# Kernel optimization log

Measured on AMD Instinct MI355X. Metric: run time of the kernel, lower is better.

The kernel has to match this reference:

```python
import jax, jax.numpy as jnp
import numpy as np
from jax import lax

EPS = 1e-5
PH = PW = 2  # patch size

def _bn(x, g, b, m, v):
    # eval-mode BatchNorm2d on NCHW
    scale = (g / jnp.sqrt(v + EPS))[None, :, None, None]
    return (x - m[None, :, None, None]) * scale + b[None, :, None, None]

def _gn1(x, g, b):
    # GroupNorm(num_groups=1): normalize over (C,P,N) per sample
    mu = x.mean(axis=(1, 2, 3), keepdims=True)
    var = x.var(axis=(1, 2, 3), keepdims=True)
    return (x - mu) / jnp.sqrt(var + EPS) * g[None, :, None, None] + b[None, :, None, None]

def _conv1x1(x, w, b=None):
    y = jnp.einsum('oc,bcpn->bopn', w, x)
    if b is not None:
        y = y + b[None, :, None, None]
    return y

def _silu(x):
    return x * jax.nn.sigmoid(x)

def _lin_attn(x, qkv_w, qkv_b, out_w, out_b, D):
    # x: [B, D, P, N]
    qkv = _conv1x1(x, qkv_w, qkv_b)            # [B, 2D+1, P, N]
    q = qkv[:, :1]                              # [B, 1, P, N]
    k = qkv[:, 1:1 + D]                         # [B, D, P, N]
    v = qkv[:, 1 + D:]                          # [B, D, P, N]
    scores = jax.nn.softmax(q, axis=-1)         # softmax over patches N
    ctx = jnp.sum(k * scores, axis=-1, keepdims=True)  # [B, D, P, 1]
    out = jax.nn.relu(v) * ctx
    return _conv1x1(out, out_w, out_b)

def reference(x, dw_w, dw_bn_g, dw_bn_b, dw_bn_m, dw_bn_v, pw_w,
              gn1_g, gn1_b, qkv_w, qkv_b, out_w, out_b,
              gn2_g, gn2_b, ffn1_w, ffn1_b, ffn2_w, ffn2_b,
              gnf_g, gnf_b, proj_w, proj_bn_g, proj_bn_b, proj_bn_m, proj_bn_v):
    B, C, H, W = x.shape
    D = pw_w.shape[0]
    L = gn1_g.shape[0]
    # local representation: depthwise 3x3 conv + BN + SiLU, then 1x1 to attn dim
    y = lax.conv_general_dilated(x, dw_w, (1, 1), 'SAME',
                                 feature_group_count=C,
                                 dimension_numbers=('NCHW', 'OIHW', 'NCHW'))
    y = _silu(_bn(y, dw_bn_g, dw_bn_b, dw_bn_m, dw_bn_v))
    y = _conv1x1(y, pw_w)                       # [B, D, H, W]
    # unfold to [B, D, P, N] (non-overlapping patches, torch F.unfold ordering)
    nH, nW = H // PH, W // PW
    p = y.reshape(B, D, nH, PH, nW, PW).transpose(0, 1, 3, 5, 2, 4).reshape(B, D, PH * PW, nH * nW)
    # global representation: L pre-norm linear-attention + FFN blocks
    for i in range(L):
        p = p + _lin_attn(_gn1(p, gn1_g[i], gn1_b[i]), qkv_w[i], qkv_b[i], out_w[i], out_b[i], D)
        h = _gn1(p, gn2_g[i], gn2_b[i])
        h = _silu(_conv1x1(h, ffn1_w[i], ffn1_b[i]))
        h = _conv1x1(h, ffn2_w[i], ffn2_b[i])
        p = p + h
    p = _gn1(p, gnf_g, gnf_b)
    # fold back to [B, D, H, W]
    y = p.reshape(B, D, PH, PW, nH, nW).transpose(0, 1, 4, 2, 5, 3).reshape(B, D, H, W)
    # projection back to in_channels: 1x1 conv + BN (no act)
    y = _conv1x1(y, proj_w)
    y = _bn(y, proj_bn_g, proj_bn_b, proj_bn_m, proj_bn_v)
    return y

def setup_inputs() -> dict:
    key = jax.random.key(0)
    ks = iter(jax.random.split(key, 40))
    def rn(shape, s=0.05):
        return jax.random.normal(next(ks), shape, jnp.float32) * s
    B, C, H, W, D, F, L = 16, 256, 64, 64, 256, 512, 2
    return dict(
        x=jax.random.normal(next(ks), (B, C, H, W), jnp.float32),
        dw_w=rn((C, 1, 3, 3), 0.2),
        dw_bn_g=jnp.ones((C,), jnp.float32), dw_bn_b=jnp.zeros((C,), jnp.float32),
        dw_bn_m=rn((C,), 0.01), dw_bn_v=jnp.ones((C,), jnp.float32),
        pw_w=rn((D, C)),
        gn1_g=jnp.ones((L, D), jnp.float32), gn1_b=jnp.zeros((L, D), jnp.float32),
        qkv_w=rn((L, 2 * D + 1, D)), qkv_b=jnp.zeros((L, 2 * D + 1), jnp.float32),
        out_w=rn((L, D, D)), out_b=jnp.zeros((L, D), jnp.float32),
        gn2_g=jnp.ones((L, D), jnp.float32), gn2_b=jnp.zeros((L, D), jnp.float32),
        ffn1_w=rn((L, F, D)), ffn1_b=jnp.zeros((L, F), jnp.float32),
        ffn2_w=rn((L, D, F)), ffn2_b=jnp.zeros((L, D), jnp.float32),
        gnf_g=jnp.ones((D,), jnp.float32), gnf_b=jnp.zeros((D,), jnp.float32),
        proj_w=rn((C, D)),
        proj_bn_g=jnp.ones((C,), jnp.float32), proj_bn_b=jnp.zeros((C,), jnp.float32),
        proj_bn_m=rn((C,), 0.01), proj_bn_v=jnp.ones((C,), jnp.float32),
    )
```

## Files before the change

### kernel.cpp

```cpp
#include <hip/hip_runtime.h>
#include <hip/hip_bf16.h>
#include <stdint.h>


#define B_    16
#define C_    256
#define D_    256
#define NPIX  4096
#define NE_PB 1048576

typedef __attribute__((ext_vector_type(8))) short  short8;
typedef __attribute__((ext_vector_type(4))) short  short4v;
typedef __attribute__((ext_vector_type(4))) float  f32x4;
typedef __attribute__((ext_vector_type(2))) float  f32x2;

__device__ __forceinline__ float b2f(short s){
  return __uint_as_float(((unsigned)(unsigned short)s) << 16);
}
__device__ __forceinline__ short f2b(float f){
  __bf16 h = (__bf16)f;
  return *(short*)&h;
}
__device__ __forceinline__ float silu_f(float x){
  float e = __builtin_amdgcn_exp2f(-1.44269504f * x);
  return x * __builtin_amdgcn_rcpf(1.f + e);
}

__device__ __forceinline__ void gld16(const short* g, short* l){
  __builtin_amdgcn_global_load_lds(
      (const __attribute__((address_space(1))) void*)g,
      (__attribute__((address_space(3))) void*)l, 16, 0, 0);
}

__device__ __forceinline__ int pi2pix(int n){
  int p = n >> 10, idx = n & 1023;
  int h = ((idx >> 5) << 1) | (p >> 1);
  int w = ((idx & 31) << 1) | (p & 1);
  return h*64 + w;
}
__device__ __forceinline__ int pix2pi(int pix){
  int h = pix >> 6, w = pix & 63;
  return ((h & 1)*2 + (w & 1))*1024 + (h >> 1)*32 + (w >> 1);
}

__global__ void cvt6_k(const float* __restrict__ s0, const float* __restrict__ s1,
                       const float* __restrict__ s2, const float* __restrict__ s3,
                       const float* __restrict__ s4, const float* __restrict__ s5,
                       const float* __restrict__ g1, const float* __restrict__ g2,
                       const float* __restrict__ gf,
                       short* __restrict__ dst, float* __restrict__ stats){
  const int i = blockIdx.x*256 + threadIdx.x;
  if (blockIdx.x == 0 && threadIdx.x < 160) stats[threadIdx.x] = 0.f;
  if (i >= 1049088) return;
  float v;
  if      (i <  65536){ v = s0[i]; }
  else if (i < 328192){ int j = i -  65536;
                        v = s1[j] * g1[(j/131328)*256 + (j & 255)]; }
  else if (i < 459264){ v = s2[i - 328192]; }
  else if (i < 721408){ int j = i - 459264;
                        v = s3[j] * g2[(j >> 17)*256 + (j & 255)]; }
  else if (i < 983552){ v = s4[i - 721408]; }
  else               { int j = i - 983552;
                        v = s5[j] * gf[j & 255]; }
  dst[i] = f2b(v);
}

__global__ void fold_k(const float* __restrict__ qkvw, const float* __restrict__ f1w,
                       const float* __restrict__ pjw,
                       const float* __restrict__ g1, const float* __restrict__ b1,
                       const float* __restrict__ g2, const float* __restrict__ b2,
                       const float* __restrict__ gf, const float* __restrict__ bf,
                       float* __restrict__ uv){
  const int row = blockIdx.x;
  const int l = threadIdx.x;
  const float* W; const float* g; const float* bb;
  if (row < 1026){ int layer = row/513, o = row - layer*513;
    W = qkvw + (size_t)(layer*513 + o)*256; g = g1 + layer*256; bb = b1 + layer*256; }
  else if (row < 2050){ int r2 = row - 1026; int layer = r2 >> 9, o = r2 & 511;
    W = f1w + (size_t)(layer*512 + o)*256; g = g2 + layer*256; bb = b2 + layer*256; }
  else { int o = row - 2050; W = pjw + (size_t)o*256; g = gf; bb = bf; }
  float u = 0.f, v = 0.f;
#pragma unroll
  for (int k = 0; k < 4; ++k){
    const int c = l + k*64;
    const float w = W[c];
    u += w * g[c]; v += w * bb[c];
  }
#pragma unroll
  for (int o = 32; o > 0; o >>= 1){ u += __shfl_down(u, o); v += __shfl_down(v, o); }
  if (l == 0){ uv[row*2] = u; uv[row*2+1] = v; }
}

__global__ __launch_bounds__(256)
void dwconv_k(const float* __restrict__ X, const float* __restrict__ W,
              const float* __restrict__ G, const float* __restrict__ Bb,
              const float* __restrict__ Mn, const float* __restrict__ Vr,
              short* __restrict__ O){
  const int c = blockIdx.x, b = blockIdx.y;
  const int t = threadIdx.x;
  __shared__ float xs[66][68];
  if (t < 132){ int r = (t >= 66) ? 65 : 0; int cc = (t >= 66) ? t-66 : t; xs[r][cc] = 0.f; }
  if (t < 128){ int r = 1 + (t & 63); int cc = (t >> 6) ? 65 : 0; xs[r][cc] = 0.f; }
  const float* xp = X + ((size_t)(b*C_ + c)) * NPIX;
#pragma unroll
  for (int it = 0; it < 4; ++it){
    const int idx = it*256 + t;
    const int row = idx >> 4, cq = idx & 15;
    f32x4 v = *(const f32x4*)&xp[row*64 + cq*4];
    xs[row+1][cq*4+1] = v.x; xs[row+1][cq*4+2] = v.y;
    xs[row+1][cq*4+3] = v.z; xs[row+1][cq*4+4] = v.w;
  }
  float wgt[9];
#pragma unroll
  for (int j = 0; j < 9; ++j) wgt[j] = W[c*9 + j];
  const float scale = G[c] * rsqrtf(Vr[c] + 1e-5f);
  const float mu = Mn[c], bb = Bb[c];
  __syncthreads();
  const int tr = t >> 4, tc = t & 15;
  float win[6][6];
#pragma unroll
  for (int dr = 0; dr < 6; ++dr){
    f32x4 a = *(const f32x4*)&xs[tr*4+dr][tc*4];
    f32x2 bq = *(const f32x2*)&xs[tr*4+dr][tc*4+4];
    win[dr][0] = a.x; win[dr][1] = a.y; win[dr][2] = a.z; win[dr][3] = a.w;
    win[dr][4] = bq.x; win[dr][5] = bq.y;
  }
  short* op = O + ((size_t)(b*C_ + c)) * NPIX;
#pragma unroll
  for (int jr = 0; jr < 4; ++jr){
    short4v o;
#pragma unroll
    for (int jc = 0; jc < 4; ++jc){
      float s = 0.f;
#pragma unroll
      for (int dh = 0; dh < 3; ++dh)
#pragma unroll
        for (int dw = 0; dw < 3; ++dw)
          s += win[jr+dh][jc+dw] * wgt[dh*3+dw];
      float y = (s - mu) * scale + bb;
      o[jc] = f2b(silu_f(y));
    }
    *(short4v*)&op[(tr*4+jr)*64 + tc*4] = o;
  }
}

__global__ void transpose_k(const short* __restrict__ I, short* __restrict__ O){
  const int s0 = blockIdx.x*64, c0 = blockIdx.y*64, b = blockIdx.z;
  const int t = threadIdx.x;
  __shared__ short tile[64][68];
  const int hi = t >> 4, lo = t & 15;
#pragma unroll
  for (int cy = 0; cy < 4; ++cy){
    const int cl = cy*16 + hi;
    short4v v = *(const short4v*)&I[((size_t)(b*C_ + c0 + cl))*NPIX + s0 + lo*4];
    tile[lo*4+0][cl] = v.x; tile[lo*4+1][cl] = v.y;
    tile[lo*4+2][cl] = v.z; tile[lo*4+3][cl] = v.w;
  }
  __syncthreads();
#pragma unroll
  for (int py = 0; py < 4; ++py){
    const int pl = py*16 + hi;
    short4v v = *(const short4v*)&tile[pl][lo*4];
    *(short4v*)&O[((size_t)(b*NPIX + s0 + pl))*C_ + c0 + lo*4] = v;
  }
}

template<int EPI, int K, int FOLD, int GATHER>
__global__ __launch_bounds__(256, 3)
void gemm_k(const short* __restrict__ Wt, const short* __restrict__ X,
            const int M,
            const float* __restrict__ bias,
            short* __restrict__ P,
            short* __restrict__ Obf,
            float* __restrict__ Of32,
            const float* __restrict__ bng, const float* __restrict__ bnb,
            const float* __restrict__ bnm, const float* __restrict__ bnv,
            float* __restrict__ st,
            const float* __restrict__ uv, const float* __restrict__ stIn)
{
  constexpr int S = K / 64;
  const int nt = blockIdx.x;
  const int ct = blockIdx.y;
  const int b  = blockIdx.z;
  const int tid = threadIdx.x;
  const int ln = tid & 63, wv = tid >> 6;
  const int wx = wv & 1;
  const int wy = wv >> 1;
  const int lr = ln & 15, lq = ln >> 4;
  const int rl = ln >> 3, sp = ln & 7;
  const int sw = sp ^ rl;
  const int ch8 = (tid & 15) * 8;

  __shared__ __align__(16) char smem[33824];
  short* As = (short*)smem;
  short* Xs = (short*)(smem + 16384);
  float* CT = (float*)smem;
  float* red = (float*)(smem + 33792);

  const short* Wp = Wt + (size_t)(ct*128)*K;
  const short* Xp = X + ((size_t)b*NPIX + (size_t)nt*128) * K;

  const short* gw[4]; const short* gx[4]; short* lw[4]; short* lx[4];
#pragma unroll
  for (int j = 0; j < 4; ++j){
    const int row = 32*wv + 8*j + rl;
    gw[j] = Wp + (size_t)row*K + sw*8;
    if constexpr (GATHER == 1)
      gx[j] = X + ((size_t)b*NPIX + pi2pix(nt*128 + row))*K + sw*8;
    else if constexpr (GATHER == 2)
      gx[j] = X + ((size_t)b*NPIX + pix2pi(nt*128 + row))*K + sw*8;
    else
      gx[j] = Xp + (size_t)row*K + sw*8;
    lw[j] = As + (4*wv + j)*512;
    lx[j] = Xs + (4*wv + j)*512;
  }

  short8 oldv[2][4];
  if constexpr (EPI == 2){
#pragma unroll
    for (int p = 0; p < 2; ++p)
#pragma unroll
      for (int it = 0; it < 4; ++it){
        const int pixL = it*16 + (tid >> 4);
        const size_t rowb = (size_t)b*NPIX + nt*128 + p*64 + pixL;
        oldv[p][it] = *(const short8*)&P[rowb*256 + ct*128 + ch8];
      }
  }

  f32x4 acc[4][4];
#pragma unroll
  for (int r = 0; r < 4; ++r)
#pragma unroll
    for (int c = 0; c < 4; ++c) acc[r][c] = (f32x4){0.f,0.f,0.f,0.f};

  for (int stp = 0; stp < S; ++stp){
    if (stp) __syncthreads();
#pragma unroll
    for (int j = 0; j < 4; ++j) gld16(gw[j] + stp*64, lw[j]);
#pragma unroll
    for (int j = 0; j < 4; ++j) gld16(gx[j] + stp*64, lx[j]);
    __syncthreads();
#pragma unroll
    for (int kk = 0; kk < 2; ++kk){
      const int seg = ((kk*4 + lq) ^ (lr & 7)) * 16;
      short8 aw[4], bx[4];
#pragma unroll
      for (int r = 0; r < 4; ++r)
        aw[r] = *(const short8*)((const char*)As + (wx*64 + r*16 + lr)*128 + seg);
#pragma unroll
      for (int c = 0; c < 4; ++c)
        bx[c] = *(const short8*)((const char*)Xs + (wy*64 + c*16 + lr)*128 + seg);
#pragma unroll
      for (int r = 0; r < 4; ++r)
#pragma unroll
        for (int c = 0; c < 4; ++c)
          acc[r][c] = __builtin_amdgcn_mfma_f32_16x16x32_bf16(aw[r], bx[c], acc[r][c], 0, 0, 0);
    }
  }

  float s_mul = 1.f;
  f32x4 be0 = (f32x4){0.f,0.f,0.f,0.f}, be1 = be0;
  if constexpr (EPI == 1 || EPI == 2 || EPI == 3){
    if constexpr (!FOLD){
      be0 = *(const f32x4*)&bias[ct*128 + ch8];
      be1 = *(const f32x4*)&bias[ct*128 + ch8 + 4];
    }
  }
  if constexpr (FOLD && EPI != 4){
    const float mean = stIn[b*2]   * (1.f/NE_PB);
    const float m2   = stIn[b*2+1] * (1.f/NE_PB);
    const float inv  = rsqrtf(m2 - mean*mean + 1e-5f);
    s_mul = inv;
    const float muinv = mean * inv;
    const float* up = &uv[(size_t)(ct*128 + ch8)*2];
#pragma unroll
    for (int k = 0; k < 4; ++k){
      f32x2 p0 = *(const f32x2*)&up[k*2];
      f32x2 p1 = *(const f32x2*)&up[8 + k*2];
      be0[k] += p0.y - muinv*p0.x;
      be1[k] += p1.y - muinv*p1.x;
    }
    if constexpr (EPI == 1 || EPI == 2 || EPI == 3){
      if (bias){
        f32x4 bb0 = *(const f32x4*)&bias[ct*128 + ch8];
        f32x4 bb1 = *(const f32x4*)&bias[ct*128 + ch8 + 4];
        be0.x += bb0.x; be0.y += bb0.y; be0.z += bb0.z; be0.w += bb0.w;
        be1.x += bb1.x; be1.y += bb1.y; be1.z += bb1.z; be1.w += bb1.w;
      }
    }
  }

  float sm = 0.f, ss = 0.f;

  if constexpr (EPI != 4){
#pragma unroll
    for (int p = 0; p < 2; ++p){
      __syncthreads();
      if (wy == p){
#pragma unroll
        for (int r = 0; r < 4; ++r)
#pragma unroll
          for (int c = 0; c < 4; ++c)
            *(f32x4*)&CT[(c*16 + lr)*132 + wx*64 + r*16 + lq*4] = acc[r][c];
      }
      __syncthreads();
#pragma unroll
      for (int it = 0; it < 4; ++it){
        const int pixL = it*16 + (tid >> 4);
        f32x4 v0 = *(const f32x4*)&CT[pixL*132 + ch8];
        f32x4 v1 = *(const f32x4*)&CT[pixL*132 + ch8 + 4];
        if constexpr (EPI != 0){
          v0.x = v0.x*s_mul + be0.x; v0.y = v0.y*s_mul + be0.y;
          v0.z = v0.z*s_mul + be0.z; v0.w = v0.w*s_mul + be0.w;
          v1.x = v1.x*s_mul + be1.x; v1.y = v1.y*s_mul + be1.y;
          v1.z = v1.z*s_mul + be1.z; v1.w = v1.w*s_mul + be1.w;
        }
        const int pixg = nt*128 + p*64 + pixL;
        const size_t rowb = (size_t)b*NPIX + pixg;
        if constexpr (EPI == 0){
          short8 o;
          o[0]=f2b(v0.x); o[1]=f2b(v0.y); o[2]=f2b(v0.z); o[3]=f2b(v0.w);
          o[4]=f2b(v1.x); o[5]=f2b(v1.y); o[6]=f2b(v1.z); o[7]=f2b(v1.w);
          *(short8*)&P[rowb*256 + ct*128 + ch8] = o;
          sm += v0.x+v0.y+v0.z+v0.w + v1.x+v1.y+v1.z+v1.w;
          ss += v0.x*v0.x+v0.y*v0.y+v0.z*v0.z+v0.w*v0.w
              + v1.x*v1.x+v1.y*v1.y+v1.z*v1.z+v1.w*v1.w;
        } else if constexpr (EPI == 2){
          short8 old = oldv[p][it];
          float n0 = b2f(old[0])+v0.x, n1 = b2f(old[1])+v0.y;
          float n2 = b2f(old[2])+v0.z, n3 = b2f(old[3])+v0.w;
          float n4 = b2f(old[4])+v1.x, n5 = b2f(old[5])+v1.y;
          float n6 = b2f(old[6])+v1.z, n7 = b2f(old[7])+v1.w;
          short8 o;
          o[0]=f2b(n0); o[1]=f2b(n1); o[2]=f2b(n2); o[3]=f2b(n3);
          o[4]=f2b(n4); o[5]=f2b(n5); o[6]=f2b(n6); o[7]=f2b(n7);
          *(short8*)&P[rowb*256 + ct*128 + ch8] = o;
          sm += n0+n1+n2+n3+n4+n5+n6+n7;
          ss += n0*n0+n1*n1+n2*n2+n3*n3+n4*n4+n5*n5+n6*n6+n7*n7;
        } else if constexpr (EPI == 1){
          short8 o;
          o[0]=f2b(v0.x); o[1]=f2b(v0.y); o[2]=f2b(v0.z); o[3]=f2b(v0.w);
          o[4]=f2b(v1.x); o[5]=f2b(v1.y); o[6]=f2b(v1.z); o[7]=f2b(v1.w);
          *(short8*)&Obf[rowb*(size_t)M + ct*128 + ch8] = o;
        } else {
          short8 o;
          o[0]=f2b(silu_f(v0.x)); o[1]=f2b(silu_f(v0.y));
          o[2]=f2b(silu_f(v0.z)); o[3]=f2b(silu_f(v0.w));
          o[4]=f2b(silu_f(v1.x)); o[5]=f2b(silu_f(v1.y));
          o[6]=f2b(silu_f(v1.z)); o[7]=f2b(silu_f(v1.w));
          *(short8*)&Obf[rowb*(size_t)M + ct*128 + ch8] = o;
        }
      }
    }
    if constexpr (EPI == 0 || EPI == 2){
#pragma unroll
      for (int o = 32; o > 0; o >>= 1){ sm += __shfl_down(sm, o); ss += __shfl_down(ss, o); }
      if (ln == 0){ red[wv*2] = sm; red[wv*2+1] = ss; }
      __syncthreads();
      if (tid == 0){
        atomicAdd(&st[b*2+0], red[0]+red[2]+red[4]+red[6]);
        atomicAdd(&st[b*2+1], red[1]+red[3]+red[5]+red[7]);
      }
    }
  } else {
    float muinv4 = 0.f;
    if constexpr (FOLD){
      const float mean = stIn[b*2]   * (1.f/NE_PB);
      const float m2   = stIn[b*2+1] * (1.f/NE_PB);
      const float inv  = rsqrtf(m2 - mean*mean + 1e-5f);
      s_mul = inv;
      muinv4 = mean * inv;
    }
#pragma unroll
    for (int p = 0; p < 2; ++p){
      __syncthreads();
      if (wx == p){
#pragma unroll
        for (int r = 0; r < 4; ++r)
#pragma unroll
          for (int c = 0; c < 4; ++c){
            const int pixL = wy*64 + c*16 + lr;
#pragma unroll
            for (int j = 0; j < 4; ++j)
              CT[(r*16 + lq*4 + j)*132 + pixL] = acc[r][c][j];
          }
      }
      __syncthreads();
#pragma unroll
      for (int it = 0; it < 8; ++it){
        const int idx = it*256 + tid;
        const int chL = idx >> 5, pq = (idx & 31)*4;
        const int chan = ct*128 + p*64 + chL;
        f32x4 v = *(const f32x4*)&CT[chL*132 + pq];
        const float sc = bng[chan] * rsqrtf(bnv[chan] + 1e-5f);
        const float mu = bnm[chan], bb = bnb[chan];
        float A = sc, Bc = -mu*sc + bb;
        if constexpr (FOLD){
          f32x2 uvp = *(const f32x2*)&uv[(size_t)chan*2];
          A = s_mul * sc;
          Bc = ((uvp.y - muinv4*uvp.x) - mu)*sc + bb;
        }
        f32x4 o;
        o.x = v.x*A + Bc; o.y = v.y*A + Bc;
        o.z = v.z*A + Bc; o.w = v.w*A + Bc;
        *(f32x4*)&Of32[((size_t)(b*C_ + chan))*NPIX + (size_t)nt*128 + pq] = o;
      }
    }
  }
}

__global__ void q_k(const short* __restrict__ P, const float* __restrict__ Wq,
                    const float* __restrict__ Gg, const float* __restrict__ Qb,
                    const float* __restrict__ uv, const float* __restrict__ stIn,
                    float* __restrict__ Q){
  const int lane = threadIdx.x & 63;
  const int pix = (blockIdx.x*256 + threadIdx.x) >> 6;
  const int b = pix >> 12;
  short4v u4 = *(const short4v*)&P[(size_t)pix*256 + lane*4];
  f32x4  w4 = *(const f32x4*)&Wq[lane*4];
  f32x4  g4 = *(const f32x4*)&Gg[lane*4];
  float s = b2f(u4.x)*w4.x*g4.x + b2f(u4.y)*w4.y*g4.y
          + b2f(u4.z)*w4.z*g4.z + b2f(u4.w)*w4.w*g4.w;
#pragma unroll
  for (int o = 32; o > 0; o >>= 1) s += __shfl_down(s, o);
  if (lane == 0){
    const float mean = stIn[b*2]   * (1.f/NE_PB);
    const float m2   = stIn[b*2+1] * (1.f/NE_PB);
    const float inv  = rsqrtf(m2 - mean*mean + 1e-5f);
    Q[pix] = inv*s + Qb[0] + uv[1] - inv*mean*uv[0];
  }
}

__global__ void softmax_k(const float* __restrict__ Q, float* __restrict__ S,
                          float* __restrict__ CT){
  const int bp = blockIdx.x;
  const int t = threadIdx.x;
  CT[bp*256 + t] = 0.f;
  float vals[4];
  float mx = -1e30f;
#pragma unroll
  for (int j = 0; j < 4; ++j){
    vals[j] = Q[bp*1024 + t + j*256];
    mx = fmaxf(mx, vals[j]);
  }
  __shared__ float red[4];
  const int lane = t & 63, wv = t >> 6;
#pragma unroll
  for (int o = 32; o > 0; o >>= 1) mx = fmaxf(mx, __shfl_down(mx, o));
  if (lane == 0) red[wv] = mx;
  __syncthreads();
  mx = fmaxf(fmaxf(red[0], red[1]), fmaxf(red[2], red[3]));
  __syncthreads();
  float sum = 0.f;
#pragma unroll
  for (int j = 0; j < 4; ++j){ vals[j] = expf(vals[j] - mx); sum += vals[j]; }
#pragma unroll
  for (int o = 32; o > 0; o >>= 1) sum += __shfl_down(sum, o);
  if (lane == 0) red[wv] = sum;
  __syncthreads();
  sum = red[0] + red[1] + red[2] + red[3];
  const float r = 1.f / sum;
#pragma unroll
  for (int j = 0; j < 4; ++j) S[bp*1024 + t + j*256] = vals[j]*r;
}

__global__ void ctx_k(const short* __restrict__ KV, const float* __restrict__ S,
                      float* __restrict__ CT){
  const int bp = blockIdx.x, ch = blockIdx.y;
  const int ln = threadIdx.x & 63, wv = threadIdx.x >> 6;
  const int j0 = ch*256 + wv*64;
  f32x4 acc = (f32x4){0.f,0.f,0.f,0.f};
  for (int jj = 0; jj < 64; jj += 4){
    f32x4 s4 = *(const f32x4*)&S[bp*1024 + j0 + jj];
#pragma unroll
    for (int u = 0; u < 4; ++u){
      short4v kv = *(const short4v*)&KV[((size_t)bp*1024 + j0 + jj + u)*512 + ln*4];
      const float s = s4[u];
      acc.x += b2f(kv.x)*s; acc.y += b2f(kv.y)*s;
      acc.z += b2f(kv.z)*s; acc.w += b2f(kv.w)*s;
    }
  }
  atomicAdd(&CT[bp*256 + ln*4 + 0], acc.x);
  atomicAdd(&CT[bp*256 + ln*4 + 1], acc.y);
  atomicAdd(&CT[bp*256 + ln*4 + 2], acc.z);
  atomicAdd(&CT[bp*256 + ln*4 + 3], acc.w);
}

__global__ void attn_in_k(const short* __restrict__ KV, const float* __restrict__ CT,
                          short* __restrict__ O){
  const size_t vid = (size_t)blockIdx.x*256 + threadIdx.x;
  const int c4 = (int)(vid & 63);
  const size_t r = vid >> 6;
  const int bp = (int)(r >> 10);
  short4v v4 = *(const short4v*)&KV[r*512 + 256 + c4*4];
  f32x4  cx = *(const f32x4*)&CT[bp*256 + c4*4];
  short4v o;
  o.x = f2b(fmaxf(b2f(v4.x), 0.f)*cx.x);
  o.y = f2b(fmaxf(b2f(v4.y), 0.f)*cx.y);
  o.z = f2b(fmaxf(b2f(v4.z), 0.f)*cx.z);
  o.w = f2b(fmaxf(b2f(v4.w), 0.f)*cx.w);
  *(short4v*)&O[r*256 + c4*4] = o;
}

extern "C" void kernel_launch(void* const* d_in, const int* in_sizes, int n_in,
                              void* d_out, int out_size, void* d_ws, size_t ws_size,
                              hipStream_t stream){
  const float* x      = (const float*)d_in[0];
  const float* dw_w   = (const float*)d_in[1];
  const float* dw_g   = (const float*)d_in[2];
  const float* dw_b   = (const float*)d_in[3];
  const float* dw_m   = (const float*)d_in[4];
  const float* dw_v   = (const float*)d_in[5];
  const float* pw_w   = (const float*)d_in[6];
  const float* gn1_g  = (const float*)d_in[7];
  const float* gn1_b  = (const float*)d_in[8];
  const float* qkv_w  = (const float*)d_in[9];
  const float* qkv_b  = (const float*)d_in[10];
  const float* out_w  = (const float*)d_in[11];
  const float* out_b  = (const float*)d_in[12];
  const float* gn2_g  = (const float*)d_in[13];
  const float* gn2_b  = (const float*)d_in[14];
  const float* ffn1_w = (const float*)d_in[15];
  const float* ffn1_b = (const float*)d_in[16];
  const float* ffn2_w = (const float*)d_in[17];
  const float* ffn2_b = (const float*)d_in[18];
  const float* gnf_g  = (const float*)d_in[19];
  const float* gnf_b  = (const float*)d_in[20];
  const float* proj_w = (const float*)d_in[21];
  const float* pbn_g  = (const float*)d_in[22];
  const float* pbn_b  = (const float*)d_in[23];
  const float* pbn_m  = (const float*)d_in[24];
  const float* pbn_v  = (const float*)d_in[25];
  float* out = (float*)d_out;

  uint8_t* w8 = (uint8_t*)d_ws;
  short* P     = (short*)(w8);
  short* bufA  = (short*)(w8 + 33554432);
  short* bufB  = (short*)(w8 + 67108864);
  short* wbase = (short*)(w8 + 134217728);
  short* w_pw  = wbase;
  short* w_qkv = wbase + 65536;
  short* w_out = wbase + 328192;
  short* w_f1  = wbase + 459264;
  short* w_f2  = wbase + 721408;
  short* w_pj  = wbase + 983552;
  float* qbuf  = (float*)(w8 + 136315904);
  float* scor  = (float*)(w8 + 136578048);
  float* ctxs  = (float*)(w8 + 136840192);
  float* stats = (float*)(w8 + 136905728);
  float* uvb   = (float*)(w8 + 136906368);

  cvt6_k<<<4098, 256, 0, stream>>>(pw_w, qkv_w, out_w, ffn1_w, ffn2_w, proj_w,
                                   gn1_g, gn2_g, gnf_g, wbase, stats);
  fold_k<<<2306, 64, 0, stream>>>(qkv_w, ffn1_w, proj_w,
                                  gn1_g, gn1_b, gn2_g, gn2_b, gnf_g, gnf_b, uvb);

  dwconv_k<<<dim3(256,16), 256, 0, stream>>>(x, dw_w, dw_g, dw_b, dw_m, dw_v, bufB);
  transpose_k<<<dim3(64,4,16), 256, 0, stream>>>(bufB, bufA);

  gemm_k<0,256,0,1><<<dim3(32,2,16), 256, 0, stream>>>(w_pw, bufA, 256, nullptr, P,
      nullptr, nullptr, nullptr, nullptr, nullptr, nullptr, stats + 0,
      nullptr, nullptr);

  for (int i = 0; i < 2; ++i){
    float* st1 = stats + (i == 0 ? 0 : 2)*32;
    q_k<<<16384, 256, 0, stream>>>(P, qkv_w + (size_t)i*513*256, gn1_g + i*256,
        qkv_b + i*513, uvb + (size_t)(i*513)*2, st1, qbuf);
    gemm_k<1,256,1,0><<<dim3(32,4,16), 256, 0, stream>>>(w_qkv + (i*513+1)*256, P, 512,
        qkv_b + i*513 + 1, nullptr, bufB, nullptr, nullptr, nullptr, nullptr, nullptr,
        nullptr, uvb + (size_t)(i*513+1)*2, st1);
    softmax_k<<<64, 256, 0, stream>>>(qbuf, scor, ctxs);
    ctx_k<<<dim3(64,4), 256, 0, stream>>>(bufB, scor, ctxs);
    attn_in_k<<<16384, 256, 0, stream>>>(bufB, ctxs, bufA);
    gemm_k<2,256,0,0><<<dim3(32,2,16), 256, 0, stream>>>(w_out + i*65536, bufA, 256,
        out_b + i*256, P, nullptr, nullptr, nullptr, nullptr, nullptr, nullptr,
        stats + (i == 0 ? 1 : 3)*32, nullptr, nullptr);
    float* st2 = stats + (i == 0 ? 1 : 3)*32;
    gemm_k<3,256,1,0><<<dim3(32,4,16), 256, 0, stream>>>(w_f1 + i*131072, P, 512,
        ffn1_b + i*512, nullptr, bufB, nullptr, nullptr, nullptr, nullptr, nullptr,
        nullptr, uvb + (size_t)(1026 + i*512)*2, st2);
    gemm_k<2,512,0,0><<<dim3(32,2,16), 256, 0, stream>>>(w_f2 + i*131072, bufB, 256,
        ffn2_b + i*256, P, nullptr, nullptr, nullptr, nullptr, nullptr, nullptr,
        stats + (i == 0 ? 2 : 4)*32, nullptr, nullptr);
  }

  gemm_k<4,256,1,2><<<dim3(32,2,16), 256, 0, stream>>>(w_pj, P, 256, nullptr,
      nullptr, nullptr, out, pbn_g, pbn_b, pbn_m, pbn_v, nullptr,
      uvb + (size_t)2050*2, stats + 4*32);

  (void)in_sizes; (void)n_in; (void)out_size; (void)ws_size;
}
```

Before: 580.0 us.

## Double-buffer GEMM LDS tiles with async global-to-LDS prefetch two stages ahead

Converts the GEMM main loop from a single LDS buffer, which loads and then syncs every K step, into a two-stage ping-pong buffer. The next tiles' global-to-LDS loads are issued while MFMAs run on the current buffer, coordinated with explicit vmcnt/lgkmcnt waits and s_barrier. The epilogue bias and GroupNorm fold computations are hoisted above the loop so their loads overlap too. LDS use doubles to 64KB and launch bounds drop to 2 blocks per CU, so occupancy falls in exchange for latency hiding.

After: 607.4 us. +4.7%, slower.

```diff
diff --git a/kernel.cpp b/kernel.cpp
--- a/kernel.cpp
+++ b/kernel.cpp
@@ -166,7 +166,7 @@
 }
 
 template<int EPI, int K, int FOLD, int GATHER>
-__global__ __launch_bounds__(256, 3)
+__global__ __launch_bounds__(256, 2)
 void gemm_k(const short* __restrict__ Wt, const short* __restrict__ X,
             const int M,
             const float* __restrict__ bias,
@@ -191,16 +191,14 @@
   const int sw = sp ^ rl;
   const int ch8 = (tid & 15) * 8;
 
-  __shared__ __align__(16) char smem[33824];
-  short* As = (short*)smem;
-  short* Xs = (short*)(smem + 16384);
+  __shared__ __align__(16) char smem[65568];
   float* CT = (float*)smem;
-  float* red = (float*)(smem + 33792);
+  float* red = (float*)(smem + 65536);
 
   const short* Wp = Wt + (size_t)(ct*128)*K;
   const short* Xp = X + ((size_t)b*NPIX + (size_t)nt*128) * K;
 
-  const short* gw[4]; const short* gx[4]; short* lw[4]; short* lx[4];
+  const short* gw[4]; const short* gx[4]; int lo4[4];
 #pragma unroll
   for (int j = 0; j < 4; ++j){
     const int row = 32*wv + 8*j + rl;
@@ -211,9 +209,17 @@
       gx[j] = X + ((size_t)b*NPIX + pix2pi(nt*128 + row))*K + sw*8;
     else
       gx[j] = Xp + (size_t)row*K + sw*8;
-    lw[j] = As + (4*wv + j)*512;
-    lx[j] = Xs + (4*wv + j)*512;
-  }
+    lo4[j] = (4*wv + j)*512;
+  }
+
+  auto stage = [&](int stp){
+    short* as = (short*)(smem + ((stp & 1) << 15));
+    short* xs = as + 8192;
+#pragma unroll
+    for (int j = 0; j < 4; ++j) gld16(gw[j] + stp*64, as + lo4[j]);
+#pragma unroll
+    for (int j = 0; j < 4; ++j) gld16(gx[j] + stp*64, xs + lo4[j]);
+  };
 
   short8 oldv[2][4];
   if constexpr (EPI == 2){
@@ -226,67 +232,77 @@
         oldv[p][it] = *(const short8*)&P[rowb*256 + ct*128 + ch8];
       }
   }
-
-  f32x4 acc[4][4];
-#pragma unroll
-  for (int r = 0; r < 4; ++r)
-#pragma unroll
-    for (int c = 0; c < 4; ++c) acc[r][c] = (f32x4){0.f,0.f,0.f,0.f};
-
-  for (int stp = 0; stp < S; ++stp){
-    if (stp) __syncthreads();
-#pragma unroll
-    for (int j = 0; j < 4; ++j) gld16(gw[j] + stp*64, lw[j]);
-#pragma unroll
-    for (int j = 0; j < 4; ++j) gld16(gx[j] + stp*64, lx[j]);
-    __syncthreads();
-#pragma unroll
-    for (int kk = 0; kk < 2; ++kk){
-      const int seg = ((kk*4 + lq) ^ (lr & 7)) * 16;
-      short8 aw[4], bx[4];
-#pragma unroll
-      for (int r = 0; r < 4; ++r)
-        aw[r] = *(const short8*)((const char*)As + (wx*64 + r*16 + lr)*128 + seg);
-#pragma unroll
-      for (int c = 0; c < 4; ++c)
-        bx[c] = *(const short8*)((const char*)Xs + (wy*64 + c*16 + lr)*128 + seg);
-#pragma unroll
-      for (int r = 0; r < 4; ++r)
-#pragma unroll
-        for (int c = 0; c < 4; ++c)
-          acc[r][c] = __builtin_amdgcn_mfma_f32_16x16x32_bf16(aw[r], bx[c], acc[r][c], 0, 0, 0);
-    }
-  }
-
   float s_mul = 1.f;
+  float muinv4 = 0.f;
   f32x4 be0 = (f32x4){0.f,0.f,0.f,0.f}, be1 = be0;
-  if constexpr (EPI == 1 || EPI == 2 || EPI == 3){
-    if constexpr (!FOLD){
-      be0 = *(const f32x4*)&bias[ct*128 + ch8];
-      be1 = *(const f32x4*)&bias[ct*128 + ch8 + 4];
-    }
-  }
-  if constexpr (FOLD && EPI != 4){
+  if constexpr ((EPI == 1 || EPI == 2 || EPI == 3) && !FOLD){
+    be0 = *(const f32x4*)&bias[ct*128 + ch8];
+    be1 = *(const f32x4*)&bias[ct*128 + ch8 + 4];
+  }
+  if constexpr (FOLD){
     const float mean = stIn[b*2]   * (1.f/NE_PB);
     const float m2   = stIn[b*2+1] * (1.f/NE_PB);
     const float inv  = rsqrtf(m2 - mean*mean + 1e-5f);
     s_mul = inv;
     const float muinv = mean * inv;
-    const float* up = &uv[(size_t)(ct*128 + ch8)*2];
-#pragma unroll
-    for (int k = 0; k < 4; ++k){
-      f32x2 p0 = *(const f32x2*)&up[k*2];
-      f32x2 p1 = *(const f32x2*)&up[8 + k*2];
-      be0[k] += p0.y - muinv*p0.x;
-      be1[k] += p1.y - muinv*p1.x;
-    }
-    if constexpr (EPI == 1 || EPI == 2 || EPI == 3){
-      if (bias){
-        f32x4 bb0 = *(const f32x4*)&bias[ct*128 + ch8];
-        f32x4 bb1 = *(const f32x4*)&bias[ct*128 + ch8 + 4];
-        be0.x += bb0.x; be0.y += bb0.y; be0.z += bb0.z; be0.w += bb0.w;
-        be1.x += bb1.x; be1.y += bb1.y; be1.z += bb1.z; be1.w += bb1.w;
-      }
+    muinv4 = muinv;
+    if constexpr (EPI != 4){
+      const float* up = &uv[(size_t)(ct*128 + ch8)*2];
+#pragma unroll
+      for (int k = 0; k < 4; ++k){
+        f32x2 p0 = *(const f32x2*)&up[k*2];
+        f32x2 p1 = *(const f32x2*)&up[8 + k*2];
+        be0[k] += p0.y - muinv*p0.x;
+        be1[k] += p1.y - muinv*p1.x;
+      }
+      if constexpr (EPI == 1 || EPI == 2 || EPI == 3){
+        if (bias){
+          f32x4 bb0 = *(const f32x4*)&bias[ct*128 + ch8];
+          f32x4 bb1 = *(const f32x4*)&bias[ct*128 + ch8 + 4];
+          be0.x += bb0.x; be0.y += bb0.y; be0.z += bb0.z; be0.w += bb0.w;
+          be1.x += bb1.x; be1.y += bb1.y; be1.z += bb1.z; be1.w += bb1.w;
+        }
+      }
+    }
+  }
+
+  f32x4 acc[4][4];
+#pragma unroll
+  for (int r = 0; r < 4; ++r)
+#pragma unroll
+    for (int c = 0; c < 4; ++c) acc[r][c] = (f32x4){0.f,0.f,0.f,0.f};
+
+  stage(0);
+  stage(1);
+  asm volatile("s_waitcnt vmcnt(8)" ::: "memory");
+  __builtin_amdgcn_s_barrier();
+
+  for (int stp = 0; stp < S; ++stp){
+    const char* asb = (const char*)smem + ((stp & 1) << 15);
+    const char* xsb = asb + 16384;
+#pragma unroll
+    for (int kk = 0; kk < 2; ++kk){
+      const int seg = ((kk*4 + lq) ^ (lr & 7)) * 16;
+      short8 aw[4], bx[4];
+#pragma unroll
+      for (int r = 0; r < 4; ++r)
+        aw[r] = *(const short8*)(asb + (wx*64 + r*16 + lr)*128 + seg);
+#pragma unroll
+      for (int c = 0; c < 4; ++c)
+        bx[c] = *(const short8*)(xsb + (wy*64 + c*16 + lr)*128 + seg);
+#pragma unroll
+      for (int r = 0; r < 4; ++r)
+#pragma unroll
+        for (int c = 0; c < 4; ++c)
+          acc[r][c] = __builtin_amdgcn_mfma_f32_16x16x32_bf16(aw[r], bx[c], acc[r][c], 0, 0, 0);
+    }
+    asm volatile("s_waitcnt lgkmcnt(0)" ::: "memory");
+    __builtin_amdgcn_s_barrier();
+    if (stp + 2 < S) stage(stp + 2);
+    if (stp + 1 < S){
+      if (stp + 2 < S) asm volatile("s_waitcnt vmcnt(8)" ::: "memory");
+      else             asm volatile("s_waitcnt vmcnt(0)" ::: "memory");
+      __builtin_amdgcn_s_barrier();
     }
   }
 
@@ -363,14 +379,6 @@
       }
     }
   } else {
-    float muinv4 = 0.f;
-    if constexpr (FOLD){
-      const float mean = stIn[b*2]   * (1.f/NE_PB);
-      const float m2   = stIn[b*2+1] * (1.f/NE_PB);
-      const float inv  = rsqrtf(m2 - mean*mean + 1e-5f);
-      s_mul = inv;
-      muinv4 = mean * inv;
-    }
 #pragma unroll
     for (int p = 0; p < 2; ++p){
       __syncthreads();
```

## Fuse FFN up and down projections into one kernel keeping hidden in LDS

Applied to the files above, without the earlier changes.

Replaces the two FFN GEMM launches with a single ffn_k kernel. Each block computes a 128-channel chunk of the hidden activation with GroupNorm folding and SiLU, stores it in shared memory, and immediately accumulates it into the down-projection, followed by the residual add and GroupNorm statistics. This removes the global-memory round trip of the 512-channel hidden tensor and one launch. The cost is fewer blocks (512 instead of 1024/2048), heavy register use from two accumulator sets, and a grid that may leave the GPU underfilled.

Result: slower. 603.4 us (+4.0%).

```diff
diff --git a/kernel.cpp b/kernel.cpp
--- a/kernel.cpp
+++ b/kernel.cpp
@@ -409,6 +409,195 @@
   }
 }
 
+__global__ __launch_bounds__(256, 2)
+void ffn_k(const short* __restrict__ Wf1, const short* __restrict__ Wf2,
+           const float* __restrict__ b1,  const float* __restrict__ b2,
+           short* __restrict__ P,
+           const float* __restrict__ uv, const float* __restrict__ stIn,
+           float* __restrict__ st)
+{
+  const int nt = blockIdx.x;
+  const int b  = blockIdx.y;
+  const int tid = threadIdx.x;
+  const int ln = tid & 63, wv = tid >> 6;
+  const int wx = wv & 1;
+  const int wy = wv >> 1;
+  const int lr = ln & 15, lq = ln >> 4;
+  const int rl = ln >> 3, sp = ln & 7;
+  const int sw = sp ^ rl;
+  const int ch8 = (tid & 15) * 8;
+
+  __shared__ __align__(16) char smem[65536];
+  short* As = (short*)smem;
+  short* Xs = (short*)(smem + 16384);
+  float* CT = (float*)smem;
+  float* red = (float*)(smem + 33792);
+
+  const short* Pt = P + ((size_t)b*NPIX + (size_t)nt*128) * 256;
+
+  int grow[4]; int lo4[4];
+#pragma unroll
+  for (int j = 0; j < 4; ++j){
+    grow[j] = 32*wv + 8*j + rl;
+    lo4[j] = (4*wv + j)*512;
+  }
+
+  const float mean = stIn[b*2]   * (1.f/NE_PB);
+  const float m2   = stIn[b*2+1] * (1.f/NE_PB);
+  const float inv  = rsqrtf(m2 - mean*mean + 1e-5f);
+  const float muinv = mean * inv;
+
+  f32x4 acc2[2][4][4];
+#pragma unroll
+  for (int d = 0; d < 2; ++d)
+#pragma unroll
+    for (int r = 0; r < 4; ++r)
+#pragma unroll
+      for (int c = 0; c < 4; ++c) acc2[d][r][c] = (f32x4){0.f,0.f,0.f,0.f};
+
+  for (int fc = 0; fc < 4; ++fc){
+    f32x4 acc1[4][4];
+#pragma unroll
+    for (int r = 0; r < 4; ++r)
+#pragma unroll
+      for (int c = 0; c < 4; ++c) acc1[r][c] = (f32x4){0.f,0.f,0.f,0.f};
+    const short* W1 = Wf1 + (size_t)(fc*128)*256;
+    for (int s = 0; s < 4; ++s){
+      __syncthreads();
+#pragma unroll
+      for (int j = 0; j < 4; ++j)
+        gld16(W1 + (size_t)grow[j]*256 + s*64 + sw*8, As + lo4[j]);
+#pragma unroll
+      for (int j = 0; j < 4; ++j)
+        gld16(Pt + (size_t)grow[j]*256 + s*64 + sw*8, Xs + lo4[j]);
+      __syncthreads();
+#pragma unroll
+      for (int kk = 0; kk < 2; ++kk){
+        const int seg = ((kk*4 + lq) ^ (lr & 7)) * 16;
+        short8 aw[4], bx[4];
+#pragma unroll
+        for (int r = 0; r < 4; ++r)
+          aw[r] = *(const short8*)((const char*)As + (wx*64 + r*16 + lr)*128 + seg);
+#pragma unroll
+        for (int c = 0; c < 4; ++c)
+          bx[c] = *(const short8*)((const char*)Xs + (wy*64 + c*16 + lr)*128 + seg);
+#pragma unroll
+        for (int r = 0; r < 4; ++r)
+#pragma unroll
+          for (int c = 0; c < 4; ++c)
+            acc1[r][c] = __builtin_amdgcn_mfma_f32_16x16x32_bf16(aw[r], bx[c], acc1[r][c], 0, 0, 0);
+      }
+    }
+    {
+      char* hkt = (char*)smem + 32768 + (wx << 14);
+      const int c16 = 2*0 + 0;  (void)c16;
+#pragma unroll
+      for (int r = 0; r < 4; ++r){
+        const int chanF = fc*128 + wx*64 + r*16 + lq*4;
+        f32x4 bb = *(const f32x4*)&b1[chanF];
+        f32x2 q0 = *(const f32x2*)&uv[(size_t)(chanF+0)*2];
+        f32x2 q1 = *(const f32x2*)&uv[(size_t)(chanF+1)*2];
+        f32x2 q2 = *(const f32x2*)&uv[(size_t)(chanF+2)*2];
+        f32x2 q3 = *(const f32x2*)&uv[(size_t)(chanF+3)*2];
+        f32x4 be;
+        be.x = bb.x + q0.y - muinv*q0.x;
+        be.y = bb.y + q1.y - muinv*q1.x;
+        be.z = bb.z + q2.y - muinv*q2.x;
+        be.w = bb.w + q3.y - muinv*q3.x;
+        const int ch16 = r*2 + (lq >> 1);
+        const int inner = (lq & 1)*8;
+#pragma unroll
+        for (int c = 0; c < 4; ++c){
+          const int pix = wy*64 + c*16 + lr;
+          f32x4 v = acc1[r][c];
+          short4v o;
+          o.x = f2b(silu_f(v.x*inv + be.x));
+          o.y = f2b(silu_f(v.y*inv + be.y));
+          o.z = f2b(silu_f(v.z*inv + be.z));
+          o.w = f2b(silu_f(v.w*inv + be.w));
+          *(short4v*)(hkt + pix*128 + ((ch16 ^ (pix & 7)) << 4) + inner) = o;
+        }
+      }
+    }
+#pragma unroll
+    for (int dh = 0; dh < 2; ++dh){
+      const short* W2 = Wf2 + (size_t)(dh*128)*512 + fc*128;
+      for (int s2 = 0; s2 < 2; ++s2){
+        __syncthreads();
+#pragma unroll
+        for (int j = 0; j < 4; ++j)
+          gld16(W2 + (size_t)grow[j]*512 + s2*64 + sw*8, As + lo4[j]);
+        __syncthreads();
+        const char* xsb = (const char*)smem + 32768 + (s2 << 14);
+#pragma unroll
+        for (int kk = 0; kk < 2; ++kk){
+          const int seg = ((kk*4 + lq) ^ (lr & 7)) * 16;
+          short8 aw[4], bx[4];
+#pragma unroll
+          for (int r = 0; r < 4; ++r)
+            aw[r] = *(const short8*)((const char*)As + (wx*64 + r*16 + lr)*128 + seg);
+#pragma unroll
+          for (int c = 0; c < 4; ++c)
+            bx[c] = *(const short8*)(xsb + (wy*64 + c*16 + lr)*128 + seg);
+#pragma unroll
+          for (int r = 0; r < 4; ++r)
+#pragma unroll
+            for (int c = 0; c < 4; ++c)
+              acc2[dh][r][c] = __builtin_amdgcn_mfma_f32_16x16x32_bf16(aw[r], bx[c], acc2[dh][r][c], 0, 0, 0);
+        }
+      }
+    }
+  }
+
+  float sm = 0.f, ss = 0.f;
+#pragma unroll
+  for (int dh = 0; dh < 2; ++dh){
+    f32x4 be20 = *(const f32x4*)&b2[dh*128 + ch8];
+    f32x4 be21 = *(const f32x4*)&b2[dh*128 + ch8 + 4];
+#pragma unroll
+    for (int p = 0; p < 2; ++p){
+      __syncthreads();
+      if (wy == p){
+#pragma unroll
+        for (int r = 0; r < 4; ++r)
+#pragma unroll
+          for (int c = 0; c < 4; ++c)
+            *(f32x4*)&CT[(c*16 + lr)*132 + wx*64 + r*16 + lq*4] = acc2[dh][r][c];
+      }
+      __syncthreads();
+#pragma unroll
+      for (int it = 0; it < 4; ++it){
+        const int pixL = it*16 + (tid >> 4);
+        f32x4 v0 = *(const f32x4*)&CT[pixL*132 + ch8];
+        f32x4 v1 = *(const f32x4*)&CT[pixL*132 + ch8 + 4];
+        v0.x += be20.x; v0.y += be20.y; v0.z += be20.z; v0.w += be20.w;
+        v1.x += be21.x; v1.y += be21.y; v1.z += be21.z; v1.w += be21.w;
+        const size_t rowb = (size_t)b*NPIX + nt*128 + p*64 + pixL;
+        short* pp = &P[rowb*256 + dh*128 + ch8];
+        short8 old = *(const short8*)pp;
+        float n0 = b2f(old[0])+v0.x, n1 = b2f(old[1])+v0.y;
+        float n2 = b2f(old[2])+v0.z, n3 = b2f(old[3])+v0.w;
+        float n4 = b2f(old[4])+v1.x, n5 = b2f(old[5])+v1.y;
+        float n6 = b2f(old[6])+v1.z, n7 = b2f(old[7])+v1.w;
+        short8 o;
+        o[0]=f2b(n0); o[1]=f2b(n1); o[2]=f2b(n2); o[3]=f2b(n3);
+        o[4]=f2b(n4); o[5]=f2b(n5); o[6]=f2b(n6); o[7]=f2b(n7);
+        *(short8*)pp = o;
+        sm += n0+n1+n2+n3+n4+n5+n6+n7;
+        ss += n0*n0+n1*n1+n2*n2+n3*n3+n4*n4+n5*n5+n6*n6+n7*n7;
+      }
+    }
+  }
+#pragma unroll
+  for (int o = 32; o > 0; o >>= 1){ sm += __shfl_down(sm, o); ss += __shfl_down(ss, o); }
+  if (ln == 0){ red[wv*2] = sm; red[wv*2+1] = ss; }
+  __syncthreads();
+  if (tid == 0){
+    atomicAdd(&st[b*2+0], red[0]+red[2]+red[4]+red[6]);
+    atomicAdd(&st[b*2+1], red[1]+red[3]+red[5]+red[7]);
+  }
+}
+
 __global__ void q_k(const short* __restrict__ P, const float* __restrict__ Wq,
                     const float* __restrict__ Gg, const float* __restrict__ Qb,
                     const float* __restrict__ uv, const float* __restrict__ stIn,
@@ -576,12 +765,10 @@
         out_b + i*256, P, nullptr, nullptr, nullptr, nullptr, nullptr, nullptr,
         stats + (i == 0 ? 1 : 3)*32, nullptr, nullptr);
     float* st2 = stats + (i == 0 ? 1 : 3)*32;
-    gemm_k<3,256,1,0><<<dim3(32,4,16), 256, 0, stream>>>(w_f1 + i*131072, P, 512,
-        ffn1_b + i*512, nullptr, bufB, nullptr, nullptr, nullptr, nullptr, nullptr,
-        nullptr, uvb + (size_t)(1026 + i*512)*2, st2);
-    gemm_k<2,512,0,0><<<dim3(32,2,16), 256, 0, stream>>>(w_f2 + i*131072, bufB, 256,
-        ffn2_b + i*256, P, nullptr, nullptr, nullptr, nullptr, nullptr, nullptr,
-        stats + (i == 0 ? 2 : 4)*32, nullptr, nullptr);
+    ffn_k<<<dim3(32,16), 256, 0, stream>>>(w_f1 + i*131072, w_f2 + i*131072,
+        ffn1_b + i*512, ffn2_b + i*256, P,
+        uvb + (size_t)(1026 + i*512)*2, st2,
+        stats + (i == 0 ? 2 : 4)*32);
   }
 
   gemm_k<4,256,1,2><<<dim3(32,2,16), 256, 0, stream>>>(w_pj, P, 256, nullptr,
```
